# Performance work log

Hardware: AMD Instinct MI355X
Metric: run time of the kernel (lower is better)

Reference implementation:

```python
import jax, jax.numpy as jnp
import numpy as np

B, N, D = 16, 512, 768
H, E = 12, 8
HD = D // H


def setup_inputs() -> dict:
    key = jax.random.key(0)
    ks = jax.random.split(key, 10)
    s = 0.02
    return {
        "x": jax.random.normal(ks[0], (B, N, D), jnp.float32),
        "gating_weights": jax.random.uniform(ks[1], (B, E), jnp.float32),
        "Wq": jax.random.normal(ks[2], (E, D, D), jnp.float32) * s,
        "bq": jax.random.normal(ks[3], (E, D), jnp.float32) * s,
        "Wk": jax.random.normal(ks[4], (E, D, D), jnp.float32) * s,
        "bk": jax.random.normal(ks[5], (E, D), jnp.float32) * s,
        "Wv": jax.random.normal(ks[6], (E, D, D), jnp.float32) * s,
        "bv": jax.random.normal(ks[7], (E, D), jnp.float32) * s,
        "Wo": jax.random.normal(ks[8], (D, D), jnp.float32) * s,
        "bo": jax.random.normal(ks[9], (D,), jnp.float32) * s,
    }


def _gated_proj(x, g, W, b):
    # sum_e g[b,e] * (x @ W_e.T + b_e)  ==  x @ (sum_e g[b,e] W_e).T + sum_e g[b,e] b_e
    # W: [E, out, in] (torch Linear layout). Fold gating into per-sample weight.
    Wc = jnp.einsum('be,eoi->boi', g, W)      # [B, out, in]
    bc = jnp.einsum('be,eo->bo', g, b)        # [B, out]
    return jnp.einsum('bni,boi->bno', x, Wc) + bc[:, None, :]


def reference(x, gating_weights, Wq, bq, Wk, bk, Wv, bv, Wo, bo):
    g = gating_weights
    Q = _gated_proj(x, g, Wq, bq)  # [B, N, D]
    K = _gated_proj(x, g, Wk, bk)
    V = _gated_proj(x, g, Wv, bv)
    Q = Q.reshape(B, N, H, HD).transpose(0, 2, 1, 3)  # [B, H, N, HD]
    K = K.reshape(B, N, H, HD).transpose(0, 2, 1, 3)
    V = V.reshape(B, N, H, HD).transpose(0, 2, 1, 3)
    scores = jnp.einsum('bhnd,bhmd->bhnm', Q, K) / jnp.sqrt(jnp.float32(HD))
    attn = jax.nn.softmax(scores, axis=-1)            # [B, H, N, N]
    ctx = jnp.einsum('bhnm,bhmd->bhnd', attn, V)
    ctx = ctx.transpose(0, 2, 1, 3).reshape(B, N, D)
    out = jnp.einsum('bnd,od->bno', ctx, Wo) + bo
    return (out, attn)
```

## Files before the change

kernel.cpp:

```cpp
#include <hip/hip_runtime.h>
#include <hip/hip_bf16.h>

#define Bc 16
#define Nc 512
#define Dc 768
#define Hc 12
#define Ec 8
#define HDc 64
#define D3 (3 * Dc)
#define ZS ((size_t)Bc * Hc * Nc * HDc)

#define NBW  (Dc * Dc / 4 / 256)
#define NBB  (Bc * Dc / 256)
#define NBWO (Dc * Dc / 8 / 256)
#define NBX  (Bc * Nc * Dc / 8 / 256)

typedef __hip_bfloat16 bf16;
typedef short bf16x8 __attribute__((ext_vector_type(8)));
typedef float f32x4 __attribute__((ext_vector_type(4)));
typedef unsigned short u16x4 __attribute__((ext_vector_type(4)));

__device__ __forceinline__ unsigned int f2bf(float f) {
    union { __hip_bfloat16 h; unsigned short u; } cv;
    cv.h = __float2bfloat16(f);
    return (unsigned int)cv.u;
}

__device__ __forceinline__ void gload16(const void* src, void* ldsDst) {
    __builtin_amdgcn_global_load_lds((const __attribute__((address_space(1))) void*)src,
                                     (__attribute__((address_space(3))) void*)ldsDst,
                                     16, 0, 0);
}

__global__ __launch_bounds__(256) void prep_kernel(const float* __restrict__ g,
                                                   const float* __restrict__ W0,
                                                   const float* __restrict__ W1,
                                                   const float* __restrict__ W2,
                                                   const float* __restrict__ b0,
                                                   const float* __restrict__ b1,
                                                   const float* __restrict__ b2,
                                                   const float* __restrict__ Wo,
                                                   const float* __restrict__ x,
                                                   bf16* __restrict__ Wc,
                                                   float* __restrict__ bc,
                                                   bf16* __restrict__ Wo_bf,
                                                   bf16* __restrict__ x_bf) {
    __shared__ float gs[Bc * Ec];
    int blk = blockIdx.x, tid = threadIdx.x;
    if (blk < 3 * NBW) {
        if (tid < Bc * Ec) gs[tid] = g[tid];
        __syncthreads();
        int t = blk / NBW;
        const float* W = (t == 0) ? W0 : ((t == 1) ? W1 : W2);
        int p = (blk - t * NBW) * 256 + tid;
        f32x4 w[Ec];
#pragma unroll
        for (int e = 0; e < Ec; ++e) w[e] = ((const f32x4*)W)[(size_t)e * (Dc * Dc / 4) + p];
        int o = p / (Dc / 4), i4 = p - o * (Dc / 4);
#pragma unroll
        for (int b = 0; b < Bc; ++b) {
            f32x4 acc = {0.f, 0.f, 0.f, 0.f};
#pragma unroll
            for (int e = 0; e < Ec; ++e) {
                float ge = gs[b * Ec + e];
                acc[0] += ge * w[e][0]; acc[1] += ge * w[e][1];
                acc[2] += ge * w[e][2]; acc[3] += ge * w[e][3];
            }
            u16x4 ov;
#pragma unroll
            for (int j = 0; j < 4; ++j) ov[j] = (unsigned short)f2bf(acc[j]);
            *(u16x4*)&Wc[((size_t)b * D3 + t * Dc + o) * Dc + i4 * 4] = ov;
        }
    } else if (blk < 3 * NBW + NBB) {
        int i = (blk - 3 * NBW) * 256 + tid;
        int b = i / Dc, o = i - b * Dc;
        const float* bs[3] = {b0, b1, b2};
#pragma unroll
        for (int t = 0; t < 3; ++t) {
            float acc = 0.f;
#pragma unroll
            for (int e = 0; e < Ec; ++e) acc += g[b * Ec + e] * bs[t][e * Dc + o];
            bc[(size_t)b * D3 + t * Dc + o] = acc;
        }
    } else if (blk < 3 * NBW + NBB + NBWO) {
        int i = (blk - 3 * NBW - NBB) * 256 + tid;
        f32x4 a = ((const f32x4*)Wo)[i * 2];
        f32x4 b = ((const f32x4*)Wo)[i * 2 + 1];
        unsigned short t[8];
#pragma unroll
        for (int j = 0; j < 4; ++j) { t[j] = (unsigned short)f2bf(a[j]); t[4 + j] = (unsigned short)f2bf(b[j]); }
        ((bf16x8*)Wo_bf)[i] = *(bf16x8*)t;
    } else {
        int i = (blk - 3 * NBW - NBB - NBWO) * 256 + tid;
        f32x4 a = ((const f32x4*)x)[i * 2];
        f32x4 b = ((const f32x4*)x)[i * 2 + 1];
        unsigned short t[8];
#pragma unroll
        for (int j = 0; j < 4; ++j) { t[j] = (unsigned short)f2bf(a[j]); t[4 + j] = (unsigned short)f2bf(b[j]); }
        ((bf16x8*)x_bf)[i] = *(bf16x8*)t;
    }
}

template<int BM, int BN, int OMODE>
__global__ __launch_bounds__(256) void gemm_mfma(const bf16* __restrict__ Ain,
                                                 const bf16* __restrict__ Bin,
                                                 void* __restrict__ Cout,
                                                 const float* __restrict__ bias,
                                                 int lda, int ldb, int ldc, int K,
                                                 long sA, long sB, long sC, int sBias) {
    constexpr int A_LDS = BM * 128;
    constexpr int B_LDS = BN * 128;
    __shared__ __align__(16) char lds[A_LDS + B_LDS];
    char* ldsA = lds;
    char* ldsB = lds + A_LDS;

    const int tid = threadIdx.x;
    const int lane = tid & 63;
    const int wave = tid >> 6;
    const int wr = wave >> 1, wc = wave & 1;
    constexpr int TM = BM / 32;
    constexpr int TN = BN / 32;
    const int m0 = blockIdx.y * BM;
    const int n0 = blockIdx.x * BN;
    const int z = blockIdx.z;
    const int mbase = wr * (BM / 2);
    const int nbase = wc * (BN / 2);

    const bf16* Ab = Ain + (size_t)z * sA;
    const bf16* Bb = Bin + (size_t)z * sB;

    f32x4 acc[TM][TN];
#pragma unroll
    for (int m = 0; m < TM; ++m)
#pragma unroll
        for (int n = 0; n < TN; ++n) acc[m][n] = f32x4{0.f, 0.f, 0.f, 0.f};

    constexpr int ACH = BM / 64;
    constexpr int BCH = BN / 64;

    for (int k0 = 0; k0 < K; k0 += 64) {
#pragma unroll
        for (int hh = 0; hh < 2; ++hh)
#pragma unroll
            for (int c = 0; c < ACH; ++c) {
                int q = wave * ACH + c;
                int row = q * 16 + (lane >> 2);
                int sl = (lane & 3) ^ (row & 3);
                const bf16* src = Ab + (size_t)(m0 + row) * lda + k0 + hh * 32 + sl * 8;
                gload16(src, ldsA + hh * (BM * 64) + q * 1024);
            }
#pragma unroll
        for (int hh = 0; hh < 2; ++hh)
#pragma unroll
            for (int c = 0; c < BCH; ++c) {
                int q = wave * BCH + c;
                int row = q * 16 + (lane >> 2);
                int sl = (lane & 3) ^ (row & 3);
                const bf16* src = Bb + (size_t)(n0 + row) * ldb + k0 + hh * 32 + sl * 8;
                gload16(src, ldsB + hh * (BN * 64) + q * 1024);
            }
        __syncthreads();

#pragma unroll
        for (int hh = 0; hh < 2; ++hh) {
            bf16x8 af[TM], bfr[TN];
#pragma unroll
            for (int m = 0; m < TM; ++m) {
                int r = mbase + m * 16 + (lane & 15);
                int sp = (lane >> 4) ^ (lane & 3);
                af[m] = *(const bf16x8*)(ldsA + hh * (BM * 64) + r * 64 + sp * 16);
            }
#pragma unroll
            for (int n = 0; n < TN; ++n) {
                int r = nbase + n * 16 + (lane & 15);
                int sp = (lane >> 4) ^ (lane & 3);
                bfr[n] = *(const bf16x8*)(ldsB + hh * (BN * 64) + r * 64 + sp * 16);
            }
#pragma unroll
            for (int m = 0; m < TM; ++m)
#pragma unroll
                for (int n = 0; n < TN; ++n)
                    acc[m][n] = __builtin_amdgcn_mfma_f32_16x16x32_bf16(af[m], bfr[n], acc[m][n], 0, 0, 0);
        }
        __syncthreads();
    }

#pragma unroll
    for (int n = 0; n < TN; ++n) {
        int colbase = n0 + nbase + n * 16;
        int col = colbase + (lane & 15);
        float bv = bias ? bias[(size_t)z * sBias + col] : 0.f;
        if constexpr (OMODE == 1) {
            int t = colbase / Dc;
            int within = colbase - t * Dc;
            int h = within >> 6;
            int dbase = within & 63;
            if (t == 2) {
                bf16* vp = (bf16*)Cout + 2 * ZS
                         + (((size_t)(z * Hc + h) * 16) * 4 + (dbase >> 4)) * 512
                         + (size_t)lane * 8;
#pragma unroll
                for (int m = 0; m < TM; ++m) {
                    int rowblk = m0 + mbase + m * 16;
                    int c = rowblk >> 5, jb = (rowblk >> 4) & 1;
                    uint2 wv = {f2bf(acc[m][n][0] + bv) | (f2bf(acc[m][n][1] + bv) << 16),
                                f2bf(acc[m][n][2] + bv) | (f2bf(acc[m][n][3] + bv) << 16)};
                    *(uint2*)(vp + (size_t)c * 2048 + jb * 4) = wv;
                }
            } else {
                float qs = (t == 0) ? 0.125f : 1.0f;
                bf16* dst = (bf16*)Cout + (size_t)t * ZS
                          + ((size_t)(z * Hc + h) * Nc) * HDc + dbase + (lane & 15);
#pragma unroll
                for (int m = 0; m < TM; ++m) {
                    int row = m0 + mbase + m * 16 + (lane >> 4) * 4;
#pragma unroll
                    for (int r = 0; r < 4; ++r)
                        dst[(size_t)(row + r) * HDc] = __float2bfloat16((acc[m][n][r] + bv) * qs);
                }
            }
        } else {
            size_t cOff = (size_t)z * sC;
#pragma unroll
            for (int m = 0; m < TM; ++m) {
                int row = m0 + mbase + m * 16 + (lane >> 4) * 4;
#pragma unroll
                for (int r = 0; r < 4; ++r)
                    __builtin_nontemporal_store(acc[m][n][r] + bv,
                        &((float*)Cout)[cOff + (size_t)(row + r) * ldc + col]);
            }
        }
    }
}

__global__ __launch_bounds__(256) void fused_attn_kernel(const bf16* __restrict__ Qz,
                                                         const bf16* __restrict__ Kz,
                                                         const bf16* __restrict__ Vp,
                                                         float* __restrict__ attn,
                                                         bf16* __restrict__ ctx) {
    __shared__ float msum[2][2][4][16];
    __shared__ __align__(16) char plds[2][16][1024];

    int L = blockIdx.x;
    int z = (L & 7) + 8 * (L >> 7);
    int qt = (L >> 3) & 15;
    int b = z / Hc, h = z - b * Hc;
    int wave = threadIdx.x >> 6, lane = threadIdx.x & 63;
    int cl = lane & 15, hi = lane >> 4;
    int qbase = qt * 32;

    const bf16* Qb = Qz + (size_t)z * Nc * HDc;
    bf16x8 qf[2][2];
#pragma unroll
    for (int t = 0; t < 2; ++t) {
        const bf16* qrow = Qb + (size_t)(qbase + t * 16 + cl) * HDc + hi * 8;
        qf[t][0] = *(const bf16x8*)(qrow);
        qf[t][1] = *(const bf16x8*)(qrow + 32);
    }

    const bf16* Vb = Vp + (size_t)z * 16 * 4 * 512;
    bf16x8 vpre[8];
#pragma unroll
    for (int c = 0; c < 8; ++c)
        vpre[c] = *(const bf16x8*)(Vb + ((c * 4 + wave) * 64 + lane) * 8);

    const bf16* Kb = Kz + ((size_t)z * Nc + wave * 128) * HDc;
    f32x4 s0[8], s1[8];
#pragma unroll
    for (int n = 0; n < 8; ++n) {
        const bf16* krow = Kb + (n * 16 + cl) * HDc + hi * 8;
        bf16x8 k0 = *(const bf16x8*)(krow);
        bf16x8 k1 = *(const bf16x8*)(krow + 32);
        f32x4 a0 = {0.f, 0.f, 0.f, 0.f};
        a0 = __builtin_amdgcn_mfma_f32_16x16x32_bf16(k0, qf[0][0], a0, 0, 0, 0);
        a0 = __builtin_amdgcn_mfma_f32_16x16x32_bf16(k1, qf[0][1], a0, 0, 0, 0);
        s0[n] = a0;
        f32x4 a1 = {0.f, 0.f, 0.f, 0.f};
        a1 = __builtin_amdgcn_mfma_f32_16x16x32_bf16(k0, qf[1][0], a1, 0, 0, 0);
        a1 = __builtin_amdgcn_mfma_f32_16x16x32_bf16(k1, qf[1][1], a1, 0, 0, 0);
        s1[n] = a1;
    }

    f32x4 mx0 = s0[0], mx1 = s1[0];
#pragma unroll
    for (int n = 1; n < 8; ++n)
#pragma unroll
        for (int r = 0; r < 4; ++r) {
            mx0[r] = fmaxf(mx0[r], s0[n][r]);
            mx1[r] = fmaxf(mx1[r], s1[n][r]);
        }
    float mw0 = fmaxf(fmaxf(mx0[0], mx0[1]), fmaxf(mx0[2], mx0[3]));
    float mw1 = fmaxf(fmaxf(mx1[0], mx1[1]), fmaxf(mx1[2], mx1[3]));
    mw0 = fmaxf(mw0, __shfl_xor(mw0, 16)); mw0 = fmaxf(mw0, __shfl_xor(mw0, 32));
    mw1 = fmaxf(mw1, __shfl_xor(mw1, 16)); mw1 = fmaxf(mw1, __shfl_xor(mw1, 32));
    if (lane < 16) { msum[0][0][wave][cl] = mw0; msum[0][1][wave][cl] = mw1; }
    __syncthreads();
    float m0 = fmaxf(fmaxf(msum[0][0][0][cl], msum[0][0][1][cl]),
                     fmaxf(msum[0][0][2][cl], msum[0][0][3][cl]));
    float m1 = fmaxf(fmaxf(msum[0][1][0][cl], msum[0][1][1][cl]),
                     fmaxf(msum[0][1][2][cl], msum[0][1][3][cl]));

    f32x4 sa0 = {0.f, 0.f, 0.f, 0.f}, sa1 = {0.f, 0.f, 0.f, 0.f};
#pragma unroll
    for (int n = 0; n < 8; ++n)
#pragma unroll
        for (int r = 0; r < 4; ++r) {
            float e0 = __expf(s0[n][r] - m0); s0[n][r] = e0; sa0[r] += e0;
            float e1 = __expf(s1[n][r] - m1); s1[n][r] = e1; sa1[r] += e1;
        }
    float sw0 = (sa0[0] + sa0[1]) + (sa0[2] + sa0[3]);
    float sw1 = (sa1[0] + sa1[1]) + (sa1[2] + sa1[3]);
    sw0 += __shfl_xor(sw0, 16); sw0 += __shfl_xor(sw0, 32);
    sw1 += __shfl_xor(sw1, 16); sw1 += __shfl_xor(sw1, 32);
    if (lane < 16) { msum[1][0][wave][cl] = sw0; msum[1][1][wave][cl] = sw1; }

    char* prow0 = plds[0][cl];
    char* prow1 = plds[1][cl];
    int swz = (cl & 7) << 4;
#pragma unroll
    for (int n = 0; n < 8; ++n) {
        int off = ((wave * 4 + (n >> 1)) * 64 + hi * 16 + (n & 1) * 8) ^ swz;
        uint2 w0v = {f2bf(s0[n][0]) | (f2bf(s0[n][1]) << 16),
                     f2bf(s0[n][2]) | (f2bf(s0[n][3]) << 16)};
        uint2 w1v = {f2bf(s1[n][0]) | (f2bf(s1[n][1]) << 16),
                     f2bf(s1[n][2]) | (f2bf(s1[n][3]) << 16)};
        *(uint2*)(prow0 + off) = w0v;
        *(uint2*)(prow1 + off) = w1v;
    }
    __syncthreads();

    float inv0 = 1.0f / ((msum[1][0][0][cl] + msum[1][0][1][cl]) +
                         (msum[1][0][2][cl] + msum[1][0][3][cl]));
    float inv1 = 1.0f / ((msum[1][1][0][cl] + msum[1][1][1][cl]) +
                         (msum[1][1][2][cl] + msum[1][1][3][cl]));

    f32x4 o0 = {0.f, 0.f, 0.f, 0.f}, o1 = {0.f, 0.f, 0.f, 0.f};
#pragma unroll
    for (int c = 0; c < 16; ++c) {
        bf16x8 vf = (c < 8) ? vpre[c]
                            : *(const bf16x8*)(Vb + ((c * 4 + wave) * 64 + lane) * 8);
        bf16x8 pf0 = *(const bf16x8*)(prow0 + ((c * 64 + hi * 16) ^ swz));
        bf16x8 pf1 = *(const bf16x8*)(prow1 + ((c * 64 + hi * 16) ^ swz));
        o0 = __builtin_amdgcn_mfma_f32_16x16x32_bf16(vf, pf0, o0, 0, 0, 0);
        o1 = __builtin_amdgcn_mfma_f32_16x16x32_bf16(vf, pf1, o1, 0, 0, 0);
    }

    bf16* cb0 = ctx + ((size_t)b * Nc + qbase + cl) * Dc + h * HDc + wave * 16;
    bf16* cb1 = cb0 + (size_t)16 * Dc;
    uint2 wv0 = {f2bf(o0[0] * inv0) | (f2bf(o0[1] * inv0) << 16),
                 f2bf(o0[2] * inv0) | (f2bf(o0[3] * inv0) << 16)};
    uint2 wv1 = {f2bf(o1[0] * inv1) | (f2bf(o1[1] * inv1) << 16),
                 f2bf(o1[2] * inv1) | (f2bf(o1[3] * inv1) << 16)};
    *(uint2*)(cb0 + hi * 4) = wv0;
    *(uint2*)(cb1 + hi * 4) = wv1;

    float* arow0 = attn + (size_t)z * Nc * Nc + (size_t)(qbase + cl) * Nc + wave * 128;
    float* arow1 = arow0 + 16 * Nc;
#pragma unroll
    for (int n = 0; n < 8; ++n) {
        f32x4 p0, p1;
#pragma unroll
        for (int r = 0; r < 4; ++r) { p0[r] = s0[n][r] * inv0; p1[r] = s1[n][r] * inv1; }
        __builtin_nontemporal_store(p0, (f32x4*)(arow0 + n * 16 + hi * 4));
        __builtin_nontemporal_store(p1, (f32x4*)(arow1 + n * 16 + hi * 4));
    }
}

extern "C" void kernel_launch(void* const* d_in, const int* in_sizes, int n_in,
                              void* d_out, int out_size, void* d_ws, size_t ws_size,
                              hipStream_t stream) {
    (void)in_sizes; (void)n_in; (void)out_size; (void)ws_size;
    const float* x  = (const float*)d_in[0];
    const float* g  = (const float*)d_in[1];
    const float* Wq = (const float*)d_in[2];
    const float* bq = (const float*)d_in[3];
    const float* Wk = (const float*)d_in[4];
    const float* bk = (const float*)d_in[5];
    const float* Wv = (const float*)d_in[6];
    const float* bv = (const float*)d_in[7];
    const float* Wo = (const float*)d_in[8];
    const float* bo = (const float*)d_in[9];

    float* out  = (float*)d_out;
    float* attn = out + (size_t)Bc * Nc * Dc;

    char* w = (char*)d_ws;
    bf16* x_bf  = (bf16*)w;
    bf16* Wo_bf = x_bf + (size_t)Bc * Nc * Dc;
    float* bc   = (float*)(Wo_bf + (size_t)Dc * Dc);
    bf16* Qz    = (bf16*)(bc + (size_t)Bc * D3);
    bf16* Kz    = Qz + ZS;
    bf16* Vp    = Qz + 2 * ZS;
    bf16* Wc    = Vp + ZS;
    bf16* ctx   = Wc;

    dim3 blk(256);

    prep_kernel<<<dim3(3 * NBW + NBB + NBWO + NBX), blk, 0, stream>>>(
        g, Wq, Wk, Wv, bq, bk, bv, Wo, x, Wc, bc, Wo_bf, x_bf);

    gemm_mfma<128, 128, 1><<<dim3(D3 / 128, Nc / 128, Bc), blk, 0, stream>>>(
        x_bf, Wc, Qz, bc, Dc, Dc, 0, Dc,
        (long)Nc * Dc, (long)D3 * Dc, 0L, D3);

    fused_attn_kernel<<<dim3(Bc * Hc * (Nc / 32)), blk, 0, stream>>>(Qz, Kz, Vp, attn, ctx);

    gemm_mfma<128, 128, 0><<<dim3(Dc / 128, Nc / 128, Bc), blk, 0, stream>>>(
        ctx, Wo_bf, out, bo, Dc, Dc, Dc, Dc,
        (long)Nc * Dc, 0L, (long)Nc * Dc, 0);
}
```

Baseline: 186.6 us.

## Remove attention max barrier via per-wave softmax rescaling; XCD-aware GEMM block mapping

In the fused attention kernel, each wave now uses its own local row max for the exponentials. The first __syncthreads for the global max is dropped, and per-wave partial sums and PV accumulators are rescaled afterwards using exp(local max − global max). This removes one block barrier and the V prefetch into registers, at the cost of extra exps and four accumulator sets. Both GEMMs switch to a 1D grid whose block index is remapped so each XCD handles two batch slices, which is meant to improve L2 locality for the per-sample weights.

```diff
diff --git a/kernel.cpp b/kernel.cpp
--- a/kernel.cpp
+++ b/kernel.cpp
@@ -101,7 +101,7 @@
     }
 }
 
-template<int BM, int BN, int OMODE>
+template<int BM, int BN, int OMODE, int NBN, int NBM>
 __global__ __launch_bounds__(256) void gemm_mfma(const bf16* __restrict__ Ain,
                                                  const bf16* __restrict__ Bin,
                                                  void* __restrict__ Cout,
@@ -120,9 +120,16 @@
     const int wr = wave >> 1, wc = wave & 1;
     constexpr int TM = BM / 32;
     constexpr int TN = BN / 32;
-    const int m0 = blockIdx.y * BM;
-    const int n0 = blockIdx.x * BN;
-    const int z = blockIdx.z;
+
+    constexpr int PERZ = NBN * NBM;
+    int L = blockIdx.x;
+    int xcd = L & 7, i = L >> 3;
+    int zi = (i >= PERZ) ? 1 : 0;
+    const int z = xcd * 2 + zi;
+    int j = i - zi * PERZ;
+    const int n0 = (j % NBN) * BN;
+    const int m0 = (j / NBN) * BM;
+
     const int mbase = wr * (BM / 2);
     const int nbase = wc * (BN / 2);
 
@@ -258,12 +265,6 @@
         qf[t][1] = *(const bf16x8*)(qrow + 32);
     }
 
-    const bf16* Vb = Vp + (size_t)z * 16 * 4 * 512;
-    bf16x8 vpre[8];
-#pragma unroll
-    for (int c = 0; c < 8; ++c)
-        vpre[c] = *(const bf16x8*)(Vb + ((c * 4 + wave) * 64 + lane) * 8);
-
     const bf16* Kb = Kz + ((size_t)z * Nc + wave * 128) * HDc;
     f32x4 s0[8], s1[8];
 #pragma unroll
@@ -293,26 +294,23 @@
     float mw1 = fmaxf(fmaxf(mx1[0], mx1[1]), fmaxf(mx1[2], mx1[3]));
     mw0 = fmaxf(mw0, __shfl_xor(mw0, 16)); mw0 = fmaxf(mw0, __shfl_xor(mw0, 32));
     mw1 = fmaxf(mw1, __shfl_xor(mw1, 16)); mw1 = fmaxf(mw1, __shfl_xor(mw1, 32));
-    if (lane < 16) { msum[0][0][wave][cl] = mw0; msum[0][1][wave][cl] = mw1; }
-    __syncthreads();
-    float m0 = fmaxf(fmaxf(msum[0][0][0][cl], msum[0][0][1][cl]),
-                     fmaxf(msum[0][0][2][cl], msum[0][0][3][cl]));
-    float m1 = fmaxf(fmaxf(msum[0][1][0][cl], msum[0][1][1][cl]),
-                     fmaxf(msum[0][1][2][cl], msum[0][1][3][cl]));
 
     f32x4 sa0 = {0.f, 0.f, 0.f, 0.f}, sa1 = {0.f, 0.f, 0.f, 0.f};
 #pragma unroll
     for (int n = 0; n < 8; ++n)
 #pragma unroll
         for (int r = 0; r < 4; ++r) {
-            float e0 = __expf(s0[n][r] - m0); s0[n][r] = e0; sa0[r] += e0;
-            float e1 = __expf(s1[n][r] - m1); s1[n][r] = e1; sa1[r] += e1;
+            float e0 = __expf(s0[n][r] - mw0); s0[n][r] = e0; sa0[r] += e0;
+            float e1 = __expf(s1[n][r] - mw1); s1[n][r] = e1; sa1[r] += e1;
         }
     float sw0 = (sa0[0] + sa0[1]) + (sa0[2] + sa0[3]);
     float sw1 = (sa1[0] + sa1[1]) + (sa1[2] + sa1[3]);
     sw0 += __shfl_xor(sw0, 16); sw0 += __shfl_xor(sw0, 32);
     sw1 += __shfl_xor(sw1, 16); sw1 += __shfl_xor(sw1, 32);
-    if (lane < 16) { msum[1][0][wave][cl] = sw0; msum[1][1][wave][cl] = sw1; }
+    if (lane < 16) {
+        msum[0][0][wave][cl] = mw0; msum[0][1][wave][cl] = mw1;
+        msum[1][0][wave][cl] = sw0; msum[1][1][wave][cl] = sw1;
+    }
 
     char* prow0 = plds[0][cl];
     char* prow1 = plds[1][cl];
@@ -329,21 +327,33 @@
     }
     __syncthreads();
 
-    float inv0 = 1.0f / ((msum[1][0][0][cl] + msum[1][0][1][cl]) +
-                         (msum[1][0][2][cl] + msum[1][0][3][cl]));
-    float inv1 = 1.0f / ((msum[1][1][0][cl] + msum[1][1][1][cl]) +
-                         (msum[1][1][2][cl] + msum[1][1][3][cl]));
-
-    f32x4 o0 = {0.f, 0.f, 0.f, 0.f}, o1 = {0.f, 0.f, 0.f, 0.f};
+    float m0 = fmaxf(fmaxf(msum[0][0][0][cl], msum[0][0][1][cl]),
+                     fmaxf(msum[0][0][2][cl], msum[0][0][3][cl]));
+    float m1 = fmaxf(fmaxf(msum[0][1][0][cl], msum[0][1][1][cl]),
+                     fmaxf(msum[0][1][2][cl], msum[0][1][3][cl]));
+    float a00 = __expf(msum[0][0][0][cl] - m0), a01 = __expf(msum[0][0][1][cl] - m0);
+    float a02 = __expf(msum[0][0][2][cl] - m0), a03 = __expf(msum[0][0][3][cl] - m0);
+    float a10 = __expf(msum[0][1][0][cl] - m1), a11 = __expf(msum[0][1][1][cl] - m1);
+    float a12 = __expf(msum[0][1][2][cl] - m1), a13 = __expf(msum[0][1][3][cl] - m1);
+    float inv0 = 1.0f / (msum[1][0][0][cl] * a00 + msum[1][0][1][cl] * a01 +
+                         msum[1][0][2][cl] * a02 + msum[1][0][3][cl] * a03);
+    float inv1 = 1.0f / (msum[1][1][0][cl] * a10 + msum[1][1][1][cl] * a11 +
+                         msum[1][1][2][cl] * a12 + msum[1][1][3][cl] * a13);
+
+    const bf16* Vb = Vp + (size_t)z * 16 * 4 * 512;
+    f32x4 o0a[4], o1a[4];
+#pragma unroll
+    for (int w = 0; w < 4; ++w) { o0a[w] = f32x4{0.f, 0.f, 0.f, 0.f}; o1a[w] = f32x4{0.f, 0.f, 0.f, 0.f}; }
 #pragma unroll
     for (int c = 0; c < 16; ++c) {
-        bf16x8 vf = (c < 8) ? vpre[c]
-                            : *(const bf16x8*)(Vb + ((c * 4 + wave) * 64 + lane) * 8);
+        bf16x8 vf = *(const bf16x8*)(Vb + ((c * 4 + wave) * 64 + lane) * 8);
         bf16x8 pf0 = *(const bf16x8*)(prow0 + ((c * 64 + hi * 16) ^ swz));
         bf16x8 pf1 = *(const bf16x8*)(prow1 + ((c * 64 + hi * 16) ^ swz));
-        o0 = __builtin_amdgcn_mfma_f32_16x16x32_bf16(vf, pf0, o0, 0, 0, 0);
-        o1 = __builtin_amdgcn_mfma_f32_16x16x32_bf16(vf, pf1, o1, 0, 0, 0);
-    }
+        o0a[c >> 2] = __builtin_amdgcn_mfma_f32_16x16x32_bf16(vf, pf0, o0a[c >> 2], 0, 0, 0);
+        o1a[c >> 2] = __builtin_amdgcn_mfma_f32_16x16x32_bf16(vf, pf1, o1a[c >> 2], 0, 0, 0);
+    }
+    f32x4 o0 = o0a[0] * a00 + o0a[1] * a01 + o0a[2] * a02 + o0a[3] * a03;
+    f32x4 o1 = o1a[0] * a10 + o1a[1] * a11 + o1a[2] * a12 + o1a[3] * a13;
 
     bf16* cb0 = ctx + ((size_t)b * Nc + qbase + cl) * Dc + h * HDc + wave * 16;
     bf16* cb1 = cb0 + (size_t)16 * Dc;
@@ -354,13 +364,15 @@
     *(uint2*)(cb0 + hi * 4) = wv0;
     *(uint2*)(cb1 + hi * 4) = wv1;
 
+    float mw0g = __expf(mw0 - m0) * inv0;
+    float mw1g = __expf(mw1 - m1) * inv1;
     float* arow0 = attn + (size_t)z * Nc * Nc + (size_t)(qbase + cl) * Nc + wave * 128;
     float* arow1 = arow0 + 16 * Nc;
 #pragma unroll
     for (int n = 0; n < 8; ++n) {
         f32x4 p0, p1;
 #pragma unroll
-        for (int r = 0; r < 4; ++r) { p0[r] = s0[n][r] * inv0; p1[r] = s1[n][r] * inv1; }
+        for (int r = 0; r < 4; ++r) { p0[r] = s0[n][r] * mw0g; p1[r] = s1[n][r] * mw1g; }
         __builtin_nontemporal_store(p0, (f32x4*)(arow0 + n * 16 + hi * 4));
         __builtin_nontemporal_store(p1, (f32x4*)(arow1 + n * 16 + hi * 4));
     }
@@ -399,13 +411,13 @@
     prep_kernel<<<dim3(3 * NBW + NBB + NBWO + NBX), blk, 0, stream>>>(
         g, Wq, Wk, Wv, bq, bk, bv, Wo, x, Wc, bc, Wo_bf, x_bf);
 
-    gemm_mfma<128, 128, 1><<<dim3(D3 / 128, Nc / 128, Bc), blk, 0, stream>>>(
+    gemm_mfma<128, 128, 1, 18, 4><<<dim3(1152), blk, 0, stream>>>(
         x_bf, Wc, Qz, bc, Dc, Dc, 0, Dc,
         (long)Nc * Dc, (long)D3 * Dc, 0L, D3);
 
     fused_attn_kernel<<<dim3(Bc * Hc * (Nc / 32)), blk, 0, stream>>>(Qz, Kz, Vp, attn, ctx);
 
-    gemm_mfma<128, 128, 0><<<dim3(Dc / 128, Nc / 128, Bc), blk, 0, stream>>>(
+    gemm_mfma<128, 128, 0, 6, 4><<<dim3(384), blk, 0, stream>>>(
         ctx, Wo_bf, out, bo, Dc, Dc, Dc, Dc,
         (long)Nc * Dc, 0L, (long)Nc * Dc, 0);
 }
```

Result: faster. 181.0 us (-3.0%).
